# Performance work log

Measured on AMD Instinct MI355X. Metric: run time of the kernel, lower is better.

The kernel has to match this reference:

```python
import jax, jax.numpy as jnp
import numpy as np

B, NV, NRINGS, NDIRS, NF = 4, 50000, 3, 16, 16


def setup_inputs() -> dict:
    key = jax.random.key(0)
    k1, k2, k3, k4 = jax.random.split(key, 4)
    basepoints = jax.random.normal(k1, (B, NV, 3), dtype=jnp.float32)
    local_frames = jax.random.normal(k2, (B, NV, 3, 3), dtype=jnp.float32)
    # expmap: gather_nd indices into basepoints' (batch, vertex) dims
    vidx = jax.random.randint(k3, (B, NV, NRINGS, NDIRS), 0, NV, dtype=jnp.int32)
    bidx = jnp.broadcast_to(jnp.arange(B, dtype=jnp.int32)[:, None, None, None],
                            (B, NV, NRINGS, NDIRS))
    expmap = jnp.stack([bidx, vidx], axis=-1)  # (B, NV, NRINGS, NDIRS, 2)
    kernel = jax.random.normal(k4, (NRINGS, NDIRS, 3, NF), dtype=jnp.float32) * 0.05
    bias = jnp.zeros((NF,), dtype=jnp.float32)
    return {"basepoints": basepoints, "local_frames": local_frames,
            "expmap": expmap, "kernel": kernel, "bias": bias}


def reference(basepoints, local_frames, expmap, kernel, bias):
    b, nv = basepoints.shape[0], basepoints.shape[1]
    nrings, ndirs = expmap.shape[2], expmap.shape[3]
    nf = kernel.shape[-1]
    # gather_nd: neighbor coordinates per (ring, direction)
    y = basepoints[expmap[..., 0], expmap[..., 1]]          # (b, nv, nrings, ndirs, 3)
    # center at basepoint
    y = y - basepoints[:, :, None, None, :]
    # rotate into local frame
    y = jnp.einsum('bvkl,bvrdl->bvrdk', local_frames, y)    # (b, nv, nrings, ndirs, 3)
    # patch conv with ring wraparound (circular padding along direction axis)
    y = y.reshape(b * nv, nrings, ndirs, 3)
    y = jnp.concatenate([y, y[:, :, :-1, :]], axis=2)       # (b*nv, nrings, 2*ndirs-1, 3)
    y = jax.lax.conv_general_dilated(
        y, kernel, window_strides=(1, 1), padding='VALID',
        dimension_numbers=('NHWC', 'HWIO', 'NHWC'))         # (b*nv, 1, ndirs, nf)
    y = y.reshape(b, nv, ndirs, nf) + bias
    return jax.nn.relu(y)
```

## Files before the change

kernel.cpp:

```cpp
#include <hip/hip_runtime.h>
#include <hip/hip_bf16.h>

#define NBATCH 4
#define NV     50000
#define VPB    16
#define VST    304

typedef __attribute__((ext_vector_type(8))) short short8;
typedef __attribute__((ext_vector_type(4))) float floatx4;

__global__ __launch_bounds__(256, 4)
void input3d_mfma(const float* __restrict__ bp,
                  const float* __restrict__ fr,
                  const int2*  __restrict__ em,
                  const float* __restrict__ kw,
                  const float* __restrict__ bias,
                  float*       __restrict__ out)
{
    __shared__ __align__(16) unsigned short yls[VPB * 2 * VST];

    const int tid  = threadIdx.x;
    const int bv0  = blockIdx.x * VPB;
    const int lane = tid & 63;
    const int wid  = tid >> 6;
    const int fcol = lane & 15;
    const int quad = lane >> 4;

    for (int i = tid; i < VPB * 51; i += 256) {
        int v = i / 51;
        int w = i - v * 51;
        int off = (w < 25) ? (279 + w) : (VST + 278 + (w - 25));
        yls[v * 2 * VST + off] = 0;
    }

    union WU { short s[8]; short8 v; };
    WU wf[5];
    #pragma unroll
    for (int kc = 0; kc < 5; ++kc) {
        #pragma unroll
        for (int j = 0; j < 8; ++j) {
            int k = kc * 32 + quad * 8 + j;
            unsigned short b = 0;
            if (k < 144) {
                int dd = k / 9;
                int q  = k - dd * 9;
                int r  = q / 3;
                int c  = q - r * 3;
                __hip_bfloat16 h = __float2bfloat16(kw[((r * 16 + dd) * 3 + c) * 16 + fcol]);
                __builtin_memcpy(&b, &h, 2);
            }
            wf[kc].s[j] = (short)b;
        }
    }
    const float bsf = bias[fcol];

    #pragma unroll
    for (int t = 0; t < 3; ++t) {
        int p   = tid + t * 256;
        int v   = p / 48;
        int i48 = p - v * 48;
        int r   = i48 >> 4;
        int dir = i48 & 15;
        int bv  = bv0 + v;
        int2 e  = em[bv * 48 + i48];
        int nb  = e.x * NV + e.y;
        float dx = bp[nb * 3 + 0] - bp[bv * 3 + 0];
        float dy = bp[nb * 3 + 1] - bp[bv * 3 + 1];
        float dz = bp[nb * 3 + 2] - bp[bv * 3 + 2];
        const float* F = fr + (size_t)bv * 9;
        unsigned short* buf = &yls[v * 2 * VST];
        #pragma unroll
        for (int c = 0; c < 3; ++c) {
            float yv = F[c * 3 + 0] * dx + F[c * 3 + 1] * dy + F[c * 3 + 2] * dz;
            __hip_bfloat16 h = __float2bfloat16(yv);
            unsigned short us;
            __builtin_memcpy(&us, &h, 2);
            int q  = r * 3 + c;
            int e1 = dir * 9 + q;
            buf[e1] = us;
            if (e1 > 0) buf[VST + e1 - 1] = us;
            if (dir < 15) {
                buf[e1 + 144] = us;
                buf[VST + e1 + 143] = us;
            }
        }
    }
    __syncthreads();

    floatx4 acc[4] = {{0.f,0.f,0.f,0.f},{0.f,0.f,0.f,0.f},
                      {0.f,0.f,0.f,0.f},{0.f,0.f,0.f,0.f}};
    const unsigned short* abase[4];
    #pragma unroll
    for (int i = 0; i < 4; ++i) {
        int v = wid * 4 + i;
        abase[i] = &yls[v * 2 * VST + ((fcol & 1) ? (VST - 1) : 0) + 9 * fcol];
    }
    #pragma unroll
    for (int kc = 0; kc < 5; ++kc) {
        const int s = kc * 32 + quad * 8;
        #pragma unroll
        for (int i = 0; i < 4; ++i) {
            const unsigned int* pa = (const unsigned int*)(abase[i] + s);
            union { unsigned int u[4]; short8 s8; } a;
            a.u[0] = pa[0]; a.u[1] = pa[1]; a.u[2] = pa[2]; a.u[3] = pa[3];
            acc[i] = __builtin_amdgcn_mfma_f32_16x16x32_bf16(a.s8, wf[kc].v, acc[i], 0, 0, 0);
        }
    }

    #pragma unroll
    for (int i = 0; i < 4; ++i) {
        int vg = bv0 + wid * 4 + i;
        float* ob = out + (size_t)vg * 256;
        #pragma unroll
        for (int rr = 0; rr < 4; ++rr) {
            float o = acc[i][rr] + bsf;
            o = o > 0.f ? o : 0.f;
            ob[(quad * 4 + rr) * 16 + fcol] = o;
        }
    }
}

extern "C" void kernel_launch(void* const* d_in, const int* in_sizes, int n_in,
                              void* d_out, int out_size, void* d_ws, size_t ws_size,
                              hipStream_t stream) {
    const float* bp   = (const float*)d_in[0];
    const float* fr   = (const float*)d_in[1];
    const int2*  em   = (const int2*)d_in[2];
    const float* kw   = (const float*)d_in[3];
    const float* bias = (const float*)d_in[4];
    float* out = (float*)d_out;

    const int total_bv = NBATCH * NV;
    const int grid = total_bv / VPB;
    input3d_mfma<<<grid, 256, 0, stream>>>(bp, fr, em, kw, bias, out);
}
```

Measured before the change: 367.4 us.

## Precompute bf16 weight fragments and restructure neighbor gather with packed LDS stores

A tiny pre-kernel converts the conv weights into per-lane bf16 MFMA fragments in workspace, so each block loads them with vector reads instead of recomputing index math and doing scattered scalar loads. The gather phase now maps one thread to one (vertex, direction), loads the frame and center once, and writes the duplicated circular-padded rows to LDS as packed 32-bit stores. The LDS zero-padding loop is removed by zeroing the A operand in registers for the last K chunk. The cost is an extra kernel launch and more registers per thread in the gather.

```diff
diff --git a/kernel.cpp b/kernel.cpp
--- a/kernel.cpp
+++ b/kernel.cpp
@@ -9,11 +9,37 @@
 typedef __attribute__((ext_vector_type(8))) short short8;
 typedef __attribute__((ext_vector_type(4))) float floatx4;
 
+__global__ void build_wfrag(const float* __restrict__ kw,
+                            unsigned short* __restrict__ wbuf) {
+    const int lane = threadIdx.x;
+    const int fcol = lane & 15;
+    const int quad = lane >> 4;
+    #pragma unroll
+    for (int kc = 0; kc < 5; ++kc) {
+        unsigned short v[8];
+        #pragma unroll
+        for (int j = 0; j < 8; ++j) {
+            int k = kc * 32 + quad * 8 + j;
+            unsigned short b = 0;
+            if (k < 144) {
+                int dd = k / 9;
+                int q  = k - dd * 9;
+                int r  = q / 3;
+                int c  = q - r * 3;
+                __hip_bfloat16 h = __float2bfloat16(kw[((r * 16 + dd) * 3 + c) * 16 + fcol]);
+                __builtin_memcpy(&b, &h, 2);
+            }
+            v[j] = b;
+        }
+        __builtin_memcpy(wbuf + lane * 40 + kc * 8, v, 16);
+    }
+}
+
 __global__ __launch_bounds__(256, 4)
 void input3d_mfma(const float* __restrict__ bp,
                   const float* __restrict__ fr,
                   const int2*  __restrict__ em,
-                  const float* __restrict__ kw,
+                  const unsigned short* __restrict__ wbuf,
                   const float* __restrict__ bias,
                   float*       __restrict__ out)
 {
@@ -26,63 +52,70 @@
     const int fcol = lane & 15;
     const int quad = lane >> 4;
 
-    for (int i = tid; i < VPB * 51; i += 256) {
-        int v = i / 51;
-        int w = i - v * 51;
-        int off = (w < 25) ? (279 + w) : (VST + 278 + (w - 25));
-        yls[v * 2 * VST + off] = 0;
-    }
-
-    union WU { short s[8]; short8 v; };
+    union WU { unsigned short s[8]; short8 v; };
     WU wf[5];
+    const unsigned short* wl = wbuf + lane * 40;
     #pragma unroll
-    for (int kc = 0; kc < 5; ++kc) {
-        #pragma unroll
-        for (int j = 0; j < 8; ++j) {
-            int k = kc * 32 + quad * 8 + j;
-            unsigned short b = 0;
-            if (k < 144) {
-                int dd = k / 9;
-                int q  = k - dd * 9;
-                int r  = q / 3;
-                int c  = q - r * 3;
-                __hip_bfloat16 h = __float2bfloat16(kw[((r * 16 + dd) * 3 + c) * 16 + fcol]);
-                __builtin_memcpy(&b, &h, 2);
-            }
-            wf[kc].s[j] = (short)b;
-        }
-    }
+    for (int kc = 0; kc < 5; ++kc)
+        __builtin_memcpy(&wf[kc].s[0], wl + kc * 8, 16);
     const float bsf = bias[fcol];
 
-    #pragma unroll
-    for (int t = 0; t < 3; ++t) {
-        int p   = tid + t * 256;
-        int v   = p / 48;
-        int i48 = p - v * 48;
-        int r   = i48 >> 4;
-        int dir = i48 & 15;
-        int bv  = bv0 + v;
-        int2 e  = em[bv * 48 + i48];
-        int nb  = e.x * NV + e.y;
-        float dx = bp[nb * 3 + 0] - bp[bv * 3 + 0];
-        float dy = bp[nb * 3 + 1] - bp[bv * 3 + 1];
-        float dz = bp[nb * 3 + 2] - bp[bv * 3 + 2];
-        const float* F = fr + (size_t)bv * 9;
+    {
+        const int v   = tid >> 4;
+        const int dir = tid & 15;
+        const int bv  = bv0 + v;
+        float F[9];
+        __builtin_memcpy(&F[0], fr + (size_t)bv * 9, 16);
+        __builtin_memcpy(&F[4], fr + (size_t)bv * 9 + 4, 16);
+        F[8] = fr[(size_t)bv * 9 + 8];
+        const float c0 = bp[bv * 3 + 0];
+        const float c1 = bp[bv * 3 + 1];
+        const float c2 = bp[bv * 3 + 2];
+
+        unsigned short val[9];
+        #pragma unroll
+        for (int r = 0; r < 3; ++r) {
+            int2 e  = em[bv * 48 + r * 16 + dir];
+            int nb  = e.x * NV + e.y;
+            float dx = bp[nb * 3 + 0] - c0;
+            float dy = bp[nb * 3 + 1] - c1;
+            float dz = bp[nb * 3 + 2] - c2;
+            #pragma unroll
+            for (int c = 0; c < 3; ++c) {
+                float yv = F[c * 3 + 0] * dx + F[c * 3 + 1] * dy + F[c * 3 + 2] * dz;
+                __hip_bfloat16 h = __float2bfloat16(yv);
+                unsigned short us;
+                __builtin_memcpy(&us, &h, 2);
+                val[r * 3 + c] = us;
+            }
+        }
+
         unsigned short* buf = &yls[v * 2 * VST];
+        unsigned int pe[4], po[4];
         #pragma unroll
-        for (int c = 0; c < 3; ++c) {
-            float yv = F[c * 3 + 0] * dx + F[c * 3 + 1] * dy + F[c * 3 + 2] * dz;
-            __hip_bfloat16 h = __float2bfloat16(yv);
-            unsigned short us;
-            __builtin_memcpy(&us, &h, 2);
-            int q  = r * 3 + c;
-            int e1 = dir * 9 + q;
-            buf[e1] = us;
-            if (e1 > 0) buf[VST + e1 - 1] = us;
-            if (dir < 15) {
-                buf[e1 + 144] = us;
-                buf[VST + e1 + 143] = us;
-            }
+        for (int i = 0; i < 4; ++i) {
+            pe[i] = (unsigned int)val[2 * i]     | ((unsigned int)val[2 * i + 1] << 16);
+            po[i] = (unsigned int)val[2 * i + 1] | ((unsigned int)val[2 * i + 2] << 16);
+        }
+        const int n0 = dir * 9;
+        auto storeE = [&](int s) {
+            unsigned int* p = (unsigned int*)(buf + s);
+            p[0] = pe[0]; p[1] = pe[1]; p[2] = pe[2]; p[3] = pe[3];
+            buf[s + 8] = val[8];
+        };
+        auto storeO = [&](int s) {
+            buf[s] = val[0];
+            unsigned int* p = (unsigned int*)(buf + s + 1);
+            p[0] = po[0]; p[1] = po[1]; p[2] = po[2]; p[3] = po[3];
+        };
+        if (dir & 1) {
+            storeO(n0);
+            storeE(VST + n0 - 1);
+            if (dir < 15) { storeO(n0 + 144); storeE(VST + n0 + 143); }
+        } else {
+            storeE(n0);
+            storeO(VST + n0 - 1);
+            if (dir < 15) { storeE(n0 + 144); storeO(VST + n0 + 143); }
         }
     }
     __syncthreads();
@@ -96,7 +129,7 @@
         abase[i] = &yls[v * 2 * VST + ((fcol & 1) ? (VST - 1) : 0) + 9 * fcol];
     }
     #pragma unroll
-    for (int kc = 0; kc < 5; ++kc) {
+    for (int kc = 0; kc < 4; ++kc) {
         const int s = kc * 32 + quad * 8;
         #pragma unroll
         for (int i = 0; i < 4; ++i) {
@@ -104,6 +137,20 @@
             union { unsigned int u[4]; short8 s8; } a;
             a.u[0] = pa[0]; a.u[1] = pa[1]; a.u[2] = pa[2]; a.u[3] = pa[3];
             acc[i] = __builtin_amdgcn_mfma_f32_16x16x32_bf16(a.s8, wf[kc].v, acc[i], 0, 0, 0);
+        }
+    }
+    {
+        const int s = 128 + quad * 8;
+        #pragma unroll
+        for (int i = 0; i < 4; ++i) {
+            union { unsigned int u[4]; short8 s8; } a;
+            if (quad < 2) {
+                const unsigned int* pa = (const unsigned int*)(abase[i] + s);
+                a.u[0] = pa[0]; a.u[1] = pa[1]; a.u[2] = pa[2]; a.u[3] = pa[3];
+            } else {
+                a.u[0] = 0; a.u[1] = 0; a.u[2] = 0; a.u[3] = 0;
+            }
+            acc[i] = __builtin_amdgcn_mfma_f32_16x16x32_bf16(a.s8, wf[4].v, acc[i], 0, 0, 0);
         }
     }
 
@@ -129,8 +176,11 @@
     const float* kw   = (const float*)d_in[3];
     const float* bias = (const float*)d_in[4];
     float* out = (float*)d_out;
+    unsigned short* wbuf = (unsigned short*)d_ws;
+
+    build_wfrag<<<1, 64, 0, stream>>>(kw, wbuf);
 
     const int total_bv = NBATCH * NV;
     const int grid = total_bv / VPB;
-    input3d_mfma<<<grid, 256, 0, stream>>>(bp, fr, em, kw, bias, out);
+    input3d_mfma<<<grid, 256, 0, stream>>>(bp, fr, em, wbuf, bias, out);
 }
```

Result: faster. 351.8 us (-4.2%).
